# Optimization experiments

Hardware: AMD Instinct MI355X
Metric: run time of the kernel (lower is better)

The kernel has to match this reference:

```python
import jax, jax.numpy as jnp
import numpy as np

SEQ_LEN, N_FEAT, EMB = 512, 8, 64
HID = 2 * EMB  # 128
BATCH = 512


def _lstm_layer(x, Wih, Whh, bih, bhh):
    """Single-layer LSTM, batch_first x: [B,T,F]. PyTorch gate order i,f,g,o.
    Returns (outputs [B,T,H], final hidden [B,H])."""
    B = x.shape[0]
    H = Whh.shape[1]
    # precompute input projections for all timesteps: [B,T,4H]
    xp = jnp.einsum('btf,gf->btg', x, Wih) + bih + bhh

    def step(carry, xt):
        h, c = carry
        gates = xt + h @ Whh.T  # [B,4H]
        i, f, g, o = jnp.split(gates, 4, axis=-1)
        i = jax.nn.sigmoid(i)
        f = jax.nn.sigmoid(f)
        g = jnp.tanh(g)
        o = jax.nn.sigmoid(o)
        c = f * c + i * g
        h = o * jnp.tanh(c)
        return (h, c), h

    h0 = jnp.zeros((B, H), dtype=x.dtype)
    c0 = jnp.zeros((B, H), dtype=x.dtype)
    (hT, _), hs = jax.lax.scan(step, (h0, c0), xp.transpose(1, 0, 2))
    return hs.transpose(1, 0, 2), hT


def setup_inputs() -> dict:
    key = jax.random.key(0)
    ks = jax.random.split(key, 13)
    inp = {"x": jax.random.normal(ks[0], (BATCH, SEQ_LEN, N_FEAT), dtype=jnp.float32)}

    def mk(k, shape, fan):
        s = 1.0 / np.sqrt(fan)
        return jax.random.uniform(k, shape, dtype=jnp.float32, minval=-s, maxval=s)

    # layer 1: in=N_FEAT, hid=HID
    inp["Wih1"] = mk(ks[1], (4 * HID, N_FEAT), HID)
    inp["Whh1"] = mk(ks[2], (4 * HID, HID), HID)
    inp["bih1"] = mk(ks[3], (4 * HID,), HID)
    inp["bhh1"] = mk(ks[4], (4 * HID,), HID)
    # layer 2: in=HID, hid=HID
    inp["Wih2"] = mk(ks[5], (4 * HID, HID), HID)
    inp["Whh2"] = mk(ks[6], (4 * HID, HID), HID)
    inp["bih2"] = mk(ks[7], (4 * HID,), HID)
    inp["bhh2"] = mk(ks[8], (4 * HID,), HID)
    # layer 3: in=HID, hid=EMB
    inp["Wih3"] = mk(ks[9], (4 * EMB, HID), EMB)
    inp["Whh3"] = mk(ks[10], (4 * EMB, EMB), EMB)
    inp["bih3"] = mk(ks[11], (4 * EMB,), EMB)
    inp["bhh3"] = mk(ks[12], (4 * EMB,), EMB)
    return inp


def reference(x, Wih1, Whh1, bih1, bhh1, Wih2, Whh2, bih2, bhh2, Wih3, Whh3, bih3, bhh3):
    B = x.shape[0]
    x = x.reshape(B, SEQ_LEN, N_FEAT)
    x, _ = _lstm_layer(x, Wih1, Whh1, bih1, bhh1)
    x, _ = _lstm_layer(x, Wih2, Whh2, bih2, bhh2)
    _, hT = _lstm_layer(x, Wih3, Whh3, bih3, bhh3)
    return hT  # [B, EMB]
```

## Files before the change

kernel.cpp:

```cpp
#include <hip/hip_runtime.h>


#define DEVI __device__ __forceinline__

typedef _Float16 h8 __attribute__((ext_vector_type(8)));
typedef float f4 __attribute__((ext_vector_type(4)));

static constexpr int T_ = 512, TC_ = 16, NC_ = T_ / TC_;

DEVI float sigmoidf_(float x) {
    return __builtin_amdgcn_rcpf(1.f + __builtin_amdgcn_exp2f(x * -1.44269504f));
}
DEVI float tanhf_(float x) {
    return 2.f * __builtin_amdgcn_rcpf(1.f + __builtin_amdgcn_exp2f(x * -2.88539008f)) - 1.f;
}

DEVI h8 cvt8(const float* p) {
    const float4 a = *reinterpret_cast<const float4*>(p);
    const float4 b = *reinterpret_cast<const float4*>(p + 4);
    return h8{(_Float16)a.x, (_Float16)a.y, (_Float16)a.z, (_Float16)a.w,
              (_Float16)b.x, (_Float16)b.y, (_Float16)b.z, (_Float16)b.w};
}

DEVI void lds_barrier() {
    asm volatile("s_waitcnt lgkmcnt(0)\n\ts_barrier" ::: "memory");
}

template <int LAYER>
DEVI void stage(int tile, char* smem, const float* x, const _Float16* Oin,
                const float* Wih, const float* Whh, const float* bih,
                const float* bhh, _Float16* Oout, float* out,
                int* flag_in, int* flag_out) {
    constexpr int H = (LAYER == 3) ? 64 : 128;
    constexpr int KT_H = H / 32;
    constexpr int KT_X = (LAYER == 1) ? 1 : 4;
    constexpr int HP = H + 8;
    constexpr int NWAVE = (LAYER == 3) ? 4 : 8;

    const int tid  = threadIdx.x;
    const int lane = tid & 63;
    const int wv   = tid >> 6;
    const int lr   = lane & 15;
    const int lk   = lane >> 4;
    const int b0   = tile * 16;
    const bool active = (wv < NWAVE);
    const int jcol = (wv & (NWAVE - 1)) * 16 + lr;

    _Float16 (*h_lds)[16][HP] = (_Float16 (*)[16][HP])smem;

    h8 wbh[4][KT_H], wbx[4][KT_X];
    float bias[4];
    if (active) {
#pragma unroll
        for (int q = 0; q < 4; q++) {
#pragma unroll
            for (int kt = 0; kt < KT_H; kt++)
                wbh[q][kt] = cvt8(Whh + (size_t)(q * H + jcol) * H + kt * 32 + lk * 8);
            if constexpr (LAYER == 1) {
                wbx[q][0] = (lk == 0) ? cvt8(Wih + (size_t)(q * H + jcol) * 8) : h8{};
            } else {
#pragma unroll
                for (int kt = 0; kt < KT_X; kt++)
                    wbx[q][kt] = cvt8(Wih + (size_t)(q * H + jcol) * 128 + kt * 32 + lk * 8);
            }
            bias[q] = bih[q * H + jcol] + bhh[q * H + jcol];
        }
    }

    float c[4] = {0.f, 0.f, 0.f, 0.f};

    for (int i = tid; i < 2 * 16 * HP; i += 512) ((_Float16*)smem)[i] = (_Float16)0;
    __syncthreads();

    auto load_x = [&](int t, h8* xa) {
        if constexpr (LAYER == 1) {
            xa[0] = (lk == 0) ? cvt8(x + ((size_t)(b0 + lr) * T_ + t) * 8) : h8{};
        } else {
#pragma unroll
            for (int kt = 0; kt < KT_X; kt++)
                xa[kt] = *reinterpret_cast<const h8*>(
                    Oin + ((size_t)(b0 + lr) * T_ + t) * 128 + kt * 32 + lk * 8);
        }
    };

    h8 xa[KT_X], xn[KT_X];

    for (int ch = 0; ch < NC_; ch++) {
        if constexpr (LAYER > 1) {
            if (tid == 0) {
                while (__hip_atomic_load(flag_in, __ATOMIC_RELAXED,
                                         __HIP_MEMORY_SCOPE_AGENT) < ch + 1)
                    __builtin_amdgcn_s_sleep(2);
                __threadfence();
            }
            __syncthreads();
        }
        if (active) load_x(ch * TC_, xa);

        for (int tt = 0; tt < TC_; tt++) {
            const int t = ch * TC_ + tt;
            const int cur = t & 1;
            if (active) {
                f4 acc[4] = {f4{0.f, 0.f, 0.f, 0.f}, f4{0.f, 0.f, 0.f, 0.f},
                             f4{0.f, 0.f, 0.f, 0.f}, f4{0.f, 0.f, 0.f, 0.f}};
#pragma unroll
                for (int kt = 0; kt < KT_X; kt++)
#pragma unroll
                    for (int q = 0; q < 4; q++)
                        acc[q] = __builtin_amdgcn_mfma_f32_16x16x32_f16(xa[kt], wbx[q][kt], acc[q], 0, 0, 0);

                if (tt + 1 < TC_) load_x(t + 1, xn);

                h8 ha[KT_H];
#pragma unroll
                for (int kt = 0; kt < KT_H; kt++)
                    ha[kt] = *reinterpret_cast<const h8*>(&h_lds[cur][lr][kt * 32 + lk * 8]);
#pragma unroll
                for (int kt = 0; kt < KT_H; kt++)
#pragma unroll
                    for (int q = 0; q < 4; q++)
                        acc[q] = __builtin_amdgcn_mfma_f32_16x16x32_f16(ha[kt], wbh[q][kt], acc[q], 0, 0, 0);

#pragma unroll
                for (int i = 0; i < 4; i++) {
                    const float gi = sigmoidf_(acc[0][i] + bias[0]);
                    const float gf = sigmoidf_(acc[1][i] + bias[1]);
                    const float gg = tanhf_(acc[2][i] + bias[2]);
                    const float go = sigmoidf_(acc[3][i] + bias[3]);
                    c[i] = gf * c[i] + gi * gg;
                    const float h = go * tanhf_(c[i]);
                    const int row = lk * 4 + i;
                    h_lds[cur ^ 1][row][jcol] = (_Float16)h;
                    if constexpr (LAYER < 3) {
                        Oout[((size_t)(b0 + row) * T_ + t) * 128 + jcol] = (_Float16)h;
                    } else {
                        if (t == T_ - 1) out[(size_t)(b0 + row) * 64 + jcol] = h;
                    }
                }
#pragma unroll
                for (int kt = 0; kt < KT_X; kt++) xa[kt] = xn[kt];
            }
            lds_barrier();
        }

        if constexpr (LAYER < 3) {
            asm volatile("s_waitcnt vmcnt(0)" ::: "memory");
            __syncthreads();
            if (tid == 0) {
                __threadfence();
                __hip_atomic_store(flag_out, ch + 1, __ATOMIC_RELAXED,
                                   __HIP_MEMORY_SCOPE_AGENT);
            }
        }
    }
}

__global__ __launch_bounds__(512, 1)
void mega_k(const float* __restrict__ x,
            const float* __restrict__ Wih1, const float* __restrict__ Whh1,
            const float* __restrict__ bih1, const float* __restrict__ bhh1,
            const float* __restrict__ Wih2, const float* __restrict__ Whh2,
            const float* __restrict__ bih2, const float* __restrict__ bhh2,
            const float* __restrict__ Wih3, const float* __restrict__ Whh3,
            const float* __restrict__ bih3, const float* __restrict__ bhh3,
            _Float16* __restrict__ O1, _Float16* __restrict__ O2,
            float* __restrict__ out, int* __restrict__ flags) {
    extern __shared__ char smem[];
    const int bid = blockIdx.x;
    if (bid < 32) {
        stage<1>(bid, smem, x, nullptr, Wih1, Whh1, bih1, bhh1, O1, nullptr,
                 nullptr, flags + bid);
    } else if (bid < 64) {
        stage<2>(bid - 32, smem, nullptr, O1, Wih2, Whh2, bih2, bhh2, O2, nullptr,
                 flags + (bid - 32), flags + 32 + (bid - 32));
    } else {
        stage<3>(bid - 64, smem, nullptr, O2, Wih3, Whh3, bih3, bhh3, nullptr, out,
                 flags + 32 + (bid - 64), nullptr);
    }
}

__global__ void zero_flags_k(int* flags) {
    if (threadIdx.x < 64)
        __hip_atomic_store(flags + threadIdx.x, 0, __ATOMIC_RELAXED,
                           __HIP_MEMORY_SCOPE_AGENT);
}

extern "C" void kernel_launch(void* const* d_in, const int* in_sizes, int n_in,
                              void* d_out, int out_size, void* d_ws, size_t ws_size,
                              hipStream_t stream) {
    const float* x    = (const float*)d_in[0];
    float* out = (float*)d_out;

    char* ws = (char*)d_ws;
    _Float16* O1 = (_Float16*)ws;
    _Float16* O2 = (_Float16*)(ws + (size_t)67108864);
    int* flags   = (int*)(ws + (size_t)134217728);
    (void)ws_size; (void)in_sizes; (void)n_in; (void)out_size;

    zero_flags_k<<<1, 64, 0, stream>>>(flags);
    mega_k<<<96, 512, 8704, stream>>>(
        x,
        (const float*)d_in[1], (const float*)d_in[2], (const float*)d_in[3], (const float*)d_in[4],
        (const float*)d_in[5], (const float*)d_in[6], (const float*)d_in[7], (const float*)d_in[8],
        (const float*)d_in[9], (const float*)d_in[10], (const float*)d_in[11], (const float*)d_in[12],
        O1, O2, out, flags);
}
```

Baseline: 845.3 us.

## Software-pipeline input projection MFMAs off the recurrent critical path

Unrolls the timestep loop by two with ping-pong accumulators so that the input-projection MFMAs for step t+1 are issued after step t's gate math, ahead of the barrier, rather than at the start of each step. The x loads are prefetched two steps ahead, and the bias is folded into the accumulator initialisation to remove per-element adds. This shortens the dependent chain between the h_lds read and the next h write, at the cost of more live registers (two accumulator sets and two x buffers) under a 512-thread, 1-block launch bound.

Measured after the change: 723.4 us. 14.4% less time.

```diff
diff --git a/kernel.cpp b/kernel.cpp
--- a/kernel.cpp
+++ b/kernel.cpp
@@ -28,8 +28,8 @@
 
 template <int LAYER>
 DEVI void stage(int tile, char* smem, const float* x, const _Float16* Oin,
-                const float* Wih, const float* Whh, const float* bih,
-                const float* bhh, _Float16* Oout, float* out,
+                _Float16* Oout, const float* Wih, const float* Whh,
+                const float* bih, const float* bhh, float* out,
                 int* flag_in, int* flag_out) {
     constexpr int H = (LAYER == 3) ? 64 : 128;
     constexpr int KT_H = H / 32;
@@ -83,7 +83,51 @@
         }
     };
 
-    h8 xa[KT_X], xn[KT_X];
+    auto xmfma = [&](const h8* xv, f4* ax) {
+#pragma unroll
+        for (int q = 0; q < 4; q++) ax[q] = f4{bias[q], bias[q], bias[q], bias[q]};
+#pragma unroll
+        for (int kt = 0; kt < KT_X; kt++)
+#pragma unroll
+            for (int q = 0; q < 4; q++)
+                ax[q] = __builtin_amdgcn_mfma_f32_16x16x32_f16(xv[kt], wbx[q][kt], ax[q], 0, 0, 0);
+    };
+
+    h8 xa[KT_X], xb[KT_X];
+    f4 accA[4], accB[4];
+
+#define STEP_BODY(T_EXPR, TT, CUR, ACCU, ACCN, XLOAD, XPROJ)                              \
+    {                                                                                     \
+        const int t = (T_EXPR);                                                           \
+        h8 ha[KT_H];                                                                      \
+        _Pragma("unroll")                                                                 \
+        for (int kt = 0; kt < KT_H; kt++)                                                 \
+            ha[kt] = *reinterpret_cast<const h8*>(&h_lds[CUR][lr][kt * 32 + lk * 8]);     \
+        _Pragma("unroll")                                                                 \
+        for (int kt = 0; kt < KT_H; kt++)                                                 \
+            _Pragma("unroll")                                                             \
+            for (int q = 0; q < 4; q++)                                                   \
+                ACCU[q] = __builtin_amdgcn_mfma_f32_16x16x32_f16(ha[kt], wbh[q][kt],      \
+                                                                 ACCU[q], 0, 0, 0);       \
+        if ((TT) + 2 < TC_) load_x(t + 2, XLOAD);          \
+        _Pragma("unroll")                                                                 \
+        for (int i = 0; i < 4; i++) {                                                     \
+            const float gi = sigmoidf_(ACCU[0][i]);                                       \
+            const float gf = sigmoidf_(ACCU[1][i]);                                       \
+            const float gg = tanhf_(ACCU[2][i]);                                          \
+            const float go = sigmoidf_(ACCU[3][i]);                                       \
+            c[i] = gf * c[i] + gi * gg;                                                   \
+            const float h = go * tanhf_(c[i]);                                            \
+            const int row = lk * 4 + i;                                                   \
+            h_lds[(CUR) ^ 1][row][jcol] = (_Float16)h;                                    \
+            if constexpr (LAYER < 3) {                                                    \
+                Oout[((size_t)(b0 + row) * T_ + t) * 128 + jcol] = (_Float16)h;           \
+            } else {                                                                      \
+                if (t == T_ - 1) out[(size_t)(b0 + row) * 64 + jcol] = h;                 \
+            }                                                                             \
+        }                                                                                 \
+        if ((TT) + 1 < TC_) xmfma(XPROJ, ACCN);   \
+    }
 
     for (int ch = 0; ch < NC_; ch++) {
         if constexpr (LAYER > 1) {
@@ -95,51 +139,17 @@
             }
             __syncthreads();
         }
-        if (active) load_x(ch * TC_, xa);
-
-        for (int tt = 0; tt < TC_; tt++) {
-            const int t = ch * TC_ + tt;
-            const int cur = t & 1;
-            if (active) {
-                f4 acc[4] = {f4{0.f, 0.f, 0.f, 0.f}, f4{0.f, 0.f, 0.f, 0.f},
-                             f4{0.f, 0.f, 0.f, 0.f}, f4{0.f, 0.f, 0.f, 0.f}};
-#pragma unroll
-                for (int kt = 0; kt < KT_X; kt++)
-#pragma unroll
-                    for (int q = 0; q < 4; q++)
-                        acc[q] = __builtin_amdgcn_mfma_f32_16x16x32_f16(xa[kt], wbx[q][kt], acc[q], 0, 0, 0);
-
-                if (tt + 1 < TC_) load_x(t + 1, xn);
-
-                h8 ha[KT_H];
-#pragma unroll
-                for (int kt = 0; kt < KT_H; kt++)
-                    ha[kt] = *reinterpret_cast<const h8*>(&h_lds[cur][lr][kt * 32 + lk * 8]);
-#pragma unroll
-                for (int kt = 0; kt < KT_H; kt++)
-#pragma unroll
-                    for (int q = 0; q < 4; q++)
-                        acc[q] = __builtin_amdgcn_mfma_f32_16x16x32_f16(ha[kt], wbh[q][kt], acc[q], 0, 0, 0);
-
-#pragma unroll
-                for (int i = 0; i < 4; i++) {
-                    const float gi = sigmoidf_(acc[0][i] + bias[0]);
-                    const float gf = sigmoidf_(acc[1][i] + bias[1]);
-                    const float gg = tanhf_(acc[2][i] + bias[2]);
-                    const float go = sigmoidf_(acc[3][i] + bias[3]);
-                    c[i] = gf * c[i] + gi * gg;
-                    const float h = go * tanhf_(c[i]);
-                    const int row = lk * 4 + i;
-                    h_lds[cur ^ 1][row][jcol] = (_Float16)h;
-                    if constexpr (LAYER < 3) {
-                        Oout[((size_t)(b0 + row) * T_ + t) * 128 + jcol] = (_Float16)h;
-                    } else {
-                        if (t == T_ - 1) out[(size_t)(b0 + row) * 64 + jcol] = h;
-                    }
-                }
-#pragma unroll
-                for (int kt = 0; kt < KT_X; kt++) xa[kt] = xn[kt];
-            }
+        const int t0 = ch * TC_;
+        if (active) {
+            load_x(t0, xa);
+            load_x(t0 + 1, xb);
+            xmfma(xa, accA);
+        }
+
+        for (int tb = 0; tb < TC_ / 2; tb++) {
+            if (active) STEP_BODY(t0 + 2 * tb, 2 * tb, 0, accA, accB, xa, xb);
+            lds_barrier();
+            if (active) STEP_BODY(t0 + 2 * tb + 1, 2 * tb + 1, 1, accB, accA, xb, xa);
             lds_barrier();
         }
 
@@ -153,6 +163,7 @@
             }
         }
     }
+#undef STEP_BODY
 }
 
 __global__ __launch_bounds__(512, 1)
@@ -168,13 +179,13 @@
     extern __shared__ char smem[];
     const int bid = blockIdx.x;
     if (bid < 32) {
-        stage<1>(bid, smem, x, nullptr, Wih1, Whh1, bih1, bhh1, O1, nullptr,
+        stage<1>(bid, smem, x, nullptr, O1, Wih1, Whh1, bih1, bhh1, nullptr,
                  nullptr, flags + bid);
     } else if (bid < 64) {
-        stage<2>(bid - 32, smem, nullptr, O1, Wih2, Whh2, bih2, bhh2, O2, nullptr,
+        stage<2>(bid - 32, smem, nullptr, O1, O2, Wih2, Whh2, bih2, bhh2, nullptr,
                  flags + (bid - 32), flags + 32 + (bid - 32));
     } else {
-        stage<3>(bid - 64, smem, nullptr, O2, Wih3, Whh3, bih3, bhh3, nullptr, out,
+        stage<3>(bid - 64, smem, nullptr, O2, nullptr, Wih3, Whh3, bih3, bhh3, out,
                  flags + 32 + (bid - 64), nullptr);
     }
 }
@@ -188,7 +199,7 @@
 extern "C" void kernel_launch(void* const* d_in, const int* in_sizes, int n_in,
                               void* d_out, int out_size, void* d_ws, size_t ws_size,
                               hipStream_t stream) {
-    const float* x    = (const float*)d_in[0];
+    const float* x = (const float*)d_in[0];
     float* out = (float*)d_out;
 
     char* ws = (char*)d_ws;
```
